# Kernel tuning notes

Hardware: AMD Instinct MI355X
Metric: run time of the kernel (lower is better)

Reference implementation:

```python
import jax, jax.numpy as jnp
import numpy as np

N, E, FIN, H, OUT, L = 80000, 1280000, 128, 64, 10, 3
NEG_SLOPE = 0.2


def setup_inputs() -> dict:
    key = jax.random.key(0)
    ks = jax.random.split(key, 2 + 6 * L + 2)
    inp = {
        "x": jax.random.normal(ks[0], (N, FIN), dtype=jnp.float32),
        "edge_index": jax.random.randint(ks[1], (2, E), 0, N, dtype=jnp.int32),
        "batch": jnp.zeros((N,), dtype=jnp.int32),
    }
    k = 2
    for l in range(L):
        fin = FIN if l == 0 else H
        s = 1.0 / np.sqrt(fin)
        inp[f"Wl{l}"] = jax.random.normal(ks[k + 0], (H, fin), dtype=jnp.float32) * s
        inp[f"bl{l}"] = jnp.zeros((H,), dtype=jnp.float32)
        inp[f"Wr{l}"] = jax.random.normal(ks[k + 1], (H, fin), dtype=jnp.float32) * s
        inp[f"br{l}"] = jnp.zeros((H,), dtype=jnp.float32)
        inp[f"att{l}"] = jax.random.normal(ks[k + 2], (H,), dtype=jnp.float32) * (1.0 / np.sqrt(H))
        inp[f"b{l}"] = jnp.zeros((H,), dtype=jnp.float32)
        k += 3
    inp["Wro"] = jax.random.normal(ks[k], (OUT, H), dtype=jnp.float32) * (1.0 / np.sqrt(H))
    inp["bro"] = jnp.zeros((OUT,), dtype=jnp.float32)
    return inp


def gatv2_layer(h, src, dst, Wl, bl, Wr, br, att, b):
    # PyG GATv2Conv (heads=1, share_weights=False):
    #   xl = lin_l(h) (source side), xr = lin_r(h) (target side)
    xl = h @ Wl.T + bl          # [N, H]
    xr = h @ Wr.T + br          # [N, H]
    e = jax.nn.leaky_relu(xl[src] + xr[dst], NEG_SLOPE) @ att  # [E_tot]
    # softmax over incoming edges of each destination node
    m = jax.ops.segment_max(e, dst, num_segments=N)
    ex = jnp.exp(e - m[dst])
    denom = jax.ops.segment_sum(ex, dst, num_segments=N)
    alpha = ex / denom[dst]
    out = jax.ops.segment_sum(alpha[:, None] * xl[src], dst, num_segments=N)
    return out + b


def reference(x, edge_index, batch,
              Wl0, bl0, Wr0, br0, att0, b0,
              Wl1, bl1, Wr1, br1, att1, b1,
              Wl2, bl2, Wr2, br2, att2, b2,
              Wro, bro):
    # add self-loops once (same augmented edge set used each layer)
    loop = jnp.arange(N, dtype=edge_index.dtype)
    src = jnp.concatenate([edge_index[0], loop])
    dst = jnp.concatenate([edge_index[1], loop])
    layers = [
        (Wl0, bl0, Wr0, br0, att0, b0),
        (Wl1, bl1, Wr1, br1, att1, b1),
        (Wl2, bl2, Wr2, br2, att2, b2),
    ]
    h = x
    for (Wl, bl, Wr, br, att, b) in layers:
        h = jax.nn.relu(gatv2_layer(h, src, dst, Wl, bl, Wr, br, att, b))
    # graph_level_task=False: node-level readout
    return h @ Wro.T + bro  # [N, OUT]
```

## Files before the change

kernel.cpp:

```cpp
#include <hip/hip_runtime.h>
#include <hip/hip_bf16.h>
#include <hip/hip_fp16.h>


#define NN 80000
#define EE 1280000
#define FIN 128
#define HH 64
#define OUTD 10
#define NBUK 79
#define PCH 2048
#define NCH 625

typedef __hip_bfloat16 bf16;

__device__ __forceinline__ float ldw(const void* p, int i, int f) {
    return f ? __bfloat162float(((const bf16*)p)[i]) : ((const float*)p)[i];
}

__global__ void detect_kernel(const unsigned* __restrict__ w, int* __restrict__ flag) {
    int lane = threadIdx.x;
    int big = 0;
    for (int i = lane; i < 2048; i += 64) {
        unsigned u = w[i];
        float a = __uint_as_float(u << 16);
        float b = __uint_as_float(u & 0xffff0000u);
        if (!(fabsf(a) <= 1024.f)) big = 1;
        if (!(fabsf(b) <= 1024.f)) big = 1;
    }
    big = (__ballot(big) != 0ull) ? 1 : 0;
    if (lane == 0) flag[0] = big ? 0 : 1;
}

__global__ void preconvert(
    const void* Wl0, const void* Wr0, const void* Wl1, const void* Wr1,
    const void* Wl2, const void* Wr2,
    const void* bl0, const void* br0, const void* bl1, const void* br1,
    const void* bl2, const void* br2,
    const void* att0, const void* att1, const void* att2,
    const void* b0, const void* b1, const void* b2,
    const void* Wro, const void* bro,
    float* WT0, float* WT1, float* WT2, float* small,
    const int* __restrict__ flagp)
{
    const int f = flagp[0];
    int t = blockIdx.x * 256 + threadIdx.x;
    if (t < 16384) {
        int j = t & 127, k = t >> 7;
        float v = (j < 64) ? ldw(Wl0, j * 128 + k, f) : ldw(Wr0, (j - 64) * 128 + k, f);
        WT0[k * 128 + j] = v;
    } else if (t < 24576) {
        int u = t - 16384; int j = u & 127, k = u >> 7;
        float v = (j < 64) ? ldw(Wl1, j * 64 + k, f) : ldw(Wr1, (j - 64) * 64 + k, f);
        WT1[k * 128 + j] = v;
    } else if (t < 32768) {
        int u = t - 24576; int j = u & 127, k = u >> 7;
        float v = (j < 64) ? ldw(Wl2, j * 64 + k, f) : ldw(Wr2, (j - 64) * 64 + k, f);
        WT2[k * 128 + j] = v;
    } else if (t < 34304) {
        int s = t - 32768;
        const void* BL[3] = { bl0, bl1, bl2 };
        const void* BR[3] = { br0, br1, br2 };
        const void* AT[3] = { att0, att1, att2 };
        const void* BB[3] = { b0, b1, b2 };
        float v = 0.f;
        if (s < 384) {
            int l = s / 128, r = s % 128;
            v = (r < 64) ? ldw(BL[l], r, f) : ldw(BR[l], r - 64, f);
        } else if (s < 576) {
            int q = s - 384; v = ldw(AT[q / 64], q % 64, f);
        } else if (s < 768) {
            int q = s - 576; v = ldw(BB[q / 64], q % 64, f);
        } else if (s < 1408) {
            v = ldw(Wro, s - 768, f);
        } else if (s < 1418) {
            v = ldw(bro, s - 1408, f);
        } else return;
        small[s] = v;
    }
}

__global__ __launch_bounds__(256) void chunkhist_kernel(const int* __restrict__ dst,
                                                        int* __restrict__ chunkcnt)
{
    __shared__ int h[NBUK];
    const int tid = threadIdx.x, c = blockIdx.x;
    for (int i = tid; i < NBUK; i += 256) h[i] = 0;
    __syncthreads();
    const int e0 = c * PCH + tid * 8;
    int4 a = *(const int4*)(dst + e0);
    int4 b = *(const int4*)(dst + e0 + 4);
    atomicAdd(&h[a.x >> 10], 1); atomicAdd(&h[a.y >> 10], 1);
    atomicAdd(&h[a.z >> 10], 1); atomicAdd(&h[a.w >> 10], 1);
    atomicAdd(&h[b.x >> 10], 1); atomicAdd(&h[b.y >> 10], 1);
    atomicAdd(&h[b.z >> 10], 1); atomicAdd(&h[b.w >> 10], 1);
    __syncthreads();
    for (int i = tid; i < NBUK; i += 256) chunkcnt[i * NCH + c] = h[i];
}

__global__ __launch_bounds__(1024) void cscan_kernel(int* __restrict__ chunkcnt,
                                                     int* __restrict__ bucket_cnt)
{
    __shared__ int s[1024];
    const int b = blockIdx.x, t = threadIdx.x;
    int v = (t < NCH) ? chunkcnt[b * NCH + t] : 0;
    s[t] = v;
    __syncthreads();
    #pragma unroll
    for (int off = 1; off < 1024; off <<= 1) {
        int u = (t >= off) ? s[t - off] : 0;
        __syncthreads();
        s[t] += u;
        __syncthreads();
    }
    if (t < NCH) chunkcnt[b * NCH + t] = s[t] - v;
    if (t == NCH - 1) bucket_cnt[b] = s[t];
}

__global__ void bscan_kernel(const int* __restrict__ bucket_cnt,
                             int* __restrict__ bucket_base)
{
    __shared__ int sc[128];
    const int t = threadIdx.x;
    sc[t] = (t < NBUK) ? bucket_cnt[t] : 0;
    __syncthreads();
    #pragma unroll
    for (int off = 1; off < 128; off <<= 1) {
        int v = (t >= off) ? sc[t - off] : 0;
        __syncthreads();
        sc[t] += v;
        __syncthreads();
    }
    if (t < NBUK) bucket_base[t] = (t == 0) ? 0 : sc[t - 1];
    if (t == 0) bucket_base[NBUK] = sc[NBUK - 1];
}

__global__ __launch_bounds__(256) void part_kernel(const int* __restrict__ src,
                                                   const int* __restrict__ dst,
                                                   const int* __restrict__ chunkcnt,
                                                   const int* __restrict__ bucket_base,
                                                   int2* __restrict__ part)
{
    __shared__ int hcnt[NBUK];
    __shared__ int sc[128];
    __shared__ int hbase[NBUK + 1];
    __shared__ int hpos[NBUK];
    __shared__ int hgb[NBUK];
    __shared__ int2 stage[PCH];
    const int tid = threadIdx.x, c = blockIdx.x;

    for (int i = tid; i < NBUK; i += 256) hcnt[i] = 0;
    __syncthreads();

    const int e0 = c * PCH + tid * 8;
    int4 sa = *(const int4*)(src + e0);
    int4 sb = *(const int4*)(src + e0 + 4);
    int4 da = *(const int4*)(dst + e0);
    int4 db = *(const int4*)(dst + e0 + 4);
    int dv[8] = { da.x, da.y, da.z, da.w, db.x, db.y, db.z, db.w };
    int sv[8] = { sa.x, sa.y, sa.z, sa.w, sb.x, sb.y, sb.z, sb.w };
    #pragma unroll
    for (int u = 0; u < 8; u++) atomicAdd(&hcnt[dv[u] >> 10], 1);
    __syncthreads();

    if (tid < 128) sc[tid] = (tid < NBUK) ? hcnt[tid] : 0;
    __syncthreads();
    #pragma unroll
    for (int off = 1; off < 128; off <<= 1) {
        int v = (tid < 128 && tid >= off) ? sc[tid - off] : 0;
        __syncthreads();
        if (tid < 128) sc[tid] += v;
        __syncthreads();
    }
    if (tid < NBUK) {
        int b = (tid == 0) ? 0 : sc[tid - 1];
        hbase[tid] = b;
        hpos[tid] = b;
        hgb[tid] = bucket_base[tid] + chunkcnt[tid * NCH + c];
    }
    if (tid == 0) hbase[NBUK] = PCH;
    __syncthreads();

    #pragma unroll
    for (int u = 0; u < 8; u++) {
        int p = atomicAdd(&hpos[dv[u] >> 10], 1);
        stage[p] = make_int2(sv[u], dv[u]);
    }
    __syncthreads();

    for (int s = tid; s < PCH; s += 256) {
        int lo = 0, hi = NBUK;
        #pragma unroll
        for (int it = 0; it < 7; it++) {
            int mid = (lo + hi) >> 1;
            if (hbase[mid] <= s) lo = mid; else hi = mid;
        }
        part[hgb[lo] + (s - hbase[lo])] = stage[s];
    }
}

__global__ __launch_bounds__(256) void hist_part_kernel(const int2* __restrict__ part,
                                                        const int* __restrict__ bucket_base,
                                                        int* __restrict__ cnt)
{
    __shared__ int lcnt[1024];
    const int b = blockIdx.x, tid = threadIdx.x;
    const int dbase = b << 10;
    for (int i = tid; i < 1024; i += 256) lcnt[i] = 0;
    __syncthreads();
    const int eb = bucket_base[b], ee = bucket_base[b + 1];
    for (int e = eb + tid; e < ee; e += 256)
        atomicAdd(&lcnt[part[e].y - dbase], 1);
    __syncthreads();
    const int nd = min(1024, NN - dbase);
    for (int i = tid; i < nd; i += 256) cnt[dbase + i] = lcnt[i];
}

__global__ void scan1(const int* __restrict__ cnt, int* __restrict__ rowptr,
                      int* __restrict__ bsums) {
    __shared__ int sh[256];
    int i = blockIdx.x * 256 + threadIdx.x;
    int tid = threadIdx.x;
    int c = (i < NN) ? cnt[i] : 0;
    sh[tid] = c;
    __syncthreads();
    #pragma unroll
    for (int off = 1; off < 256; off <<= 1) {
        int t = (tid >= off) ? sh[tid - off] : 0;
        __syncthreads();
        sh[tid] += t;
        __syncthreads();
    }
    if (i < NN) rowptr[i + 1] = sh[tid];
    if (tid == 255) bsums[blockIdx.x] = sh[255];
}

__global__ void scan2(int* __restrict__ bsums, int nb) {
    __shared__ int sh[512];
    int t = threadIdx.x;
    sh[t] = (t < nb) ? bsums[t] : 0;
    __syncthreads();
    #pragma unroll
    for (int off = 1; off < 512; off <<= 1) {
        int v = (t >= off) ? sh[t - off] : 0;
        __syncthreads();
        sh[t] += v;
        __syncthreads();
    }
    if (t < nb) bsums[t] = sh[t];
}

__global__ void scan3(int* __restrict__ rowptr, const int* __restrict__ bsums) {
    int i = blockIdx.x * 256 + threadIdx.x;
    if (i == 0) rowptr[0] = 0;
    int add = (blockIdx.x == 0) ? 0 : bsums[blockIdx.x - 1];
    if (i < NN) rowptr[i + 1] += add;
}

__global__ __launch_bounds__(256) void scatter2_kernel(const int2* __restrict__ part,
                                                       const int* __restrict__ bucket_base,
                                                       const int* __restrict__ rowptr,
                                                       int2* __restrict__ col2)
{
    __shared__ int lfill[1024];
    const int b = blockIdx.x, tid = threadIdx.x;
    const int dbase = b << 10;
    const int nd = min(1024, NN - dbase);
    for (int i = tid; i < nd; i += 256) lfill[i] = rowptr[dbase + i];
    __syncthreads();
    const int eb = bucket_base[b], ee = bucket_base[b + 1];
    for (int e = eb + tid; e < ee; e += 256) {
        int2 sd = part[e];
        int pos = atomicAdd(&lfill[sd.y - dbase], 1);
        col2[pos] = sd;
    }
}

template<int F, bool L0>
__global__ __launch_bounds__(256) void lin_fast(const void* __restrict__ hin_,
                                                const float* __restrict__ WT,
                                                const float* __restrict__ biasLR,
                                                __half* __restrict__ xlh,
                                                float* __restrict__ xr,
                                                const int* __restrict__ flagp)
{
    constexpr int LDR = 72;
    __shared__ __align__(16) float xs[F * LDR];
    const int t = threadIdx.x;
    const int nb = blockIdx.x * 64;

    if (L0 && flagp[0]) {
        const unsigned* hp = (const unsigned*)hin_;
        for (int idx = t; idx < 64 * (F / 2); idx += 256) {
            int r = idx / (F / 2), c = idx % (F / 2);
            unsigned u = hp[(size_t)(nb + r) * (F / 2) + c];
            xs[(2 * c) * LDR + r]     = __uint_as_float(u << 16);
            xs[(2 * c + 1) * LDR + r] = __uint_as_float(u & 0xffff0000u);
        }
    } else {
        const float* hp = (const float*)hin_;
        for (int idx = t; idx < 64 * F; idx += 256) {
            int r = idx / F, c = idx % F;
            xs[c * LDR + r] = hp[(size_t)(nb + r) * F + c];
        }
    }
    __syncthreads();

    const int c = t & 31;
    const int g = t >> 5;
    const float4* W4 = (const float4*)WT;
    const float4 bias = ((const float4*)biasLR)[c];
    float4 acc[8];
    #pragma unroll
    for (int u = 0; u < 8; u++) acc[u] = bias;

    #pragma unroll 2
    for (int k = 0; k < F; k++) {
        float4 w  = W4[k * 32 + c];
        float4 xa = *(const float4*)&xs[k * LDR + g * 8];
        float4 xb = *(const float4*)&xs[k * LDR + g * 8 + 4];
        acc[0].x = fmaf(xa.x, w.x, acc[0].x); acc[0].y = fmaf(xa.x, w.y, acc[0].y);
        acc[0].z = fmaf(xa.x, w.z, acc[0].z); acc[0].w = fmaf(xa.x, w.w, acc[0].w);
        acc[1].x = fmaf(xa.y, w.x, acc[1].x); acc[1].y = fmaf(xa.y, w.y, acc[1].y);
        acc[1].z = fmaf(xa.y, w.z, acc[1].z); acc[1].w = fmaf(xa.y, w.w, acc[1].w);
        acc[2].x = fmaf(xa.z, w.x, acc[2].x); acc[2].y = fmaf(xa.z, w.y, acc[2].y);
        acc[2].z = fmaf(xa.z, w.z, acc[2].z); acc[2].w = fmaf(xa.z, w.w, acc[2].w);
        acc[3].x = fmaf(xa.w, w.x, acc[3].x); acc[3].y = fmaf(xa.w, w.y, acc[3].y);
        acc[3].z = fmaf(xa.w, w.z, acc[3].z); acc[3].w = fmaf(xa.w, w.w, acc[3].w);
        acc[4].x = fmaf(xb.x, w.x, acc[4].x); acc[4].y = fmaf(xb.x, w.y, acc[4].y);
        acc[4].z = fmaf(xb.x, w.z, acc[4].z); acc[4].w = fmaf(xb.x, w.w, acc[4].w);
        acc[5].x = fmaf(xb.y, w.x, acc[5].x); acc[5].y = fmaf(xb.y, w.y, acc[5].y);
        acc[5].z = fmaf(xb.y, w.z, acc[5].z); acc[5].w = fmaf(xb.y, w.w, acc[5].w);
        acc[6].x = fmaf(xb.z, w.x, acc[6].x); acc[6].y = fmaf(xb.z, w.y, acc[6].y);
        acc[6].z = fmaf(xb.z, w.z, acc[6].z); acc[6].w = fmaf(xb.z, w.w, acc[6].w);
        acc[7].x = fmaf(xb.w, w.x, acc[7].x); acc[7].y = fmaf(xb.w, w.y, acc[7].y);
        acc[7].z = fmaf(xb.w, w.z, acc[7].z); acc[7].w = fmaf(xb.w, w.w, acc[7].w);
    }

    const int j0 = 4 * c;
    if (j0 < 64) {
        #pragma unroll
        for (int u = 0; u < 8; u++) {
            size_t row = nb + g * 8 + u;
            __half* xp = xlh + row * 64 + j0;
            *(__half2*)(xp)     = __floats2half2_rn(acc[u].x, acc[u].y);
            *(__half2*)(xp + 2) = __floats2half2_rn(acc[u].z, acc[u].w);
        }
    } else {
        #pragma unroll
        for (int u = 0; u < 8; u++) {
            size_t row = nb + g * 8 + u;
            *(float4*)(xr + row * 64 + (j0 - 64)) = acc[u];
        }
    }
}

#define DECODE8(U, D) { \
    float2 _f0 = __half22float2(*(__half2*)&U.x); \
    float2 _f1 = __half22float2(*(__half2*)&U.y); \
    float2 _f2 = __half22float2(*(__half2*)&U.z); \
    float2 _f3 = __half22float2(*(__half2*)&U.w); \
    D[0]=_f0.x; D[1]=_f0.y; D[2]=_f1.x; D[3]=_f1.y; \
    D[4]=_f2.x; D[5]=_f2.y; D[6]=_f3.x; D[7]=_f3.y; }

__global__ __launch_bounds__(256) void agg4_kernel(const __half* __restrict__ xlh,
                                                   const float* __restrict__ xr,
                                                   const float* __restrict__ attf,
                                                   const float* __restrict__ bf,
                                                   const int* __restrict__ rowptr,
                                                   const int2* __restrict__ col2,
                                                   float* __restrict__ hout)
{
    const int lane = threadIdx.x & 63;
    const int g = lane >> 3;
    const int r = lane & 7;
    int iw = blockIdx.x * 4 + (threadIdx.x >> 6);
    if (iw >= NN) return;
    const int i = __builtin_amdgcn_readfirstlane(iw);

    float xri[8], att[8];
    {
        float4 xa = *(const float4*)(xr + (size_t)i * 64 + r * 8);
        float4 xb = *(const float4*)(xr + (size_t)i * 64 + r * 8 + 4);
        xri[0]=xa.x; xri[1]=xa.y; xri[2]=xa.z; xri[3]=xa.w;
        xri[4]=xb.x; xri[5]=xb.y; xri[6]=xb.z; xri[7]=xb.w;
        float4 aa = *(const float4*)(attf + r * 8);
        float4 ab = *(const float4*)(attf + r * 8 + 4);
        att[0]=aa.x; att[1]=aa.y; att[2]=aa.z; att[3]=aa.w;
        att[4]=ab.x; att[5]=ab.y; att[6]=ab.z; att[7]=ab.w;
    }

    uint4 srow = *(const uint4*)(xlh + (size_t)i * 64 + r * 8);
    float s[8]; DECODE8(srow, s);
    float ps = 0.f;
    #pragma unroll
    for (int k = 0; k < 8; k++) {
        float u = s[k] + xri[k];
        ps = fmaf(att[k], fmaf(0.4f, fabsf(u), 0.6f * u), ps);
    }
    ps += __shfl_xor(ps, 1, 64);
    ps += __shfl_xor(ps, 2, 64);
    ps += __shfl_xor(ps, 4, 64);
    float wself = __expf(fminf(ps, 60.f));

    float acc[8];
    float denom;
    if (g == 0) {
        #pragma unroll
        for (int k = 0; k < 8; k++) acc[k] = wself * s[k];
        denom = wself;
    } else {
        #pragma unroll
        for (int k = 0; k < 8; k++) acc[k] = 0.f;
        denom = 0.f;
    }

    const int e0 = rowptr[i], e1 = rowptr[i + 1];
    const int n = e1 - e0;
    const int eL = e1 - 1;

    for (int base = 0; base < n; base += 16) {
        const int j = e0 + base;
        int sa = col2[min(j + g, eL)].x;
        int sb = col2[min(j + 8 + g, eL)].x;
        uint4 ua = *(const uint4*)(xlh + (size_t)sa * 64 + r * 8);
        uint4 ub = *(const uint4*)(xlh + (size_t)sb * 64 + r * 8);
        float A[8], B[8];
        DECODE8(ua, A);
        DECODE8(ub, B);

        float pa = 0.f, pb = 0.f;
        #pragma unroll
        for (int k = 0; k < 8; k++) {
            float va = A[k] + xri[k];
            float vb = B[k] + xri[k];
            pa = fmaf(att[k], fmaf(0.4f, fabsf(va), 0.6f * va), pa);
            pb = fmaf(att[k], fmaf(0.4f, fabsf(vb), 0.6f * vb), pb);
        }
        pa += __shfl_xor(pa, 1, 64);  pb += __shfl_xor(pb, 1, 64);
        pa += __shfl_xor(pa, 2, 64);  pb += __shfl_xor(pb, 2, 64);
        pa += __shfl_xor(pa, 4, 64);  pb += __shfl_xor(pb, 4, 64);

        float wa = (base + g < n)     ? __expf(fminf(pa, 60.f)) : 0.f;
        float wb = (base + 8 + g < n) ? __expf(fminf(pb, 60.f)) : 0.f;

        #pragma unroll
        for (int k = 0; k < 8; k++) {
            acc[k] = fmaf(wa, A[k], acc[k]);
            acc[k] = fmaf(wb, B[k], acc[k]);
        }
        denom += wa + wb;
    }

    #pragma unroll
    for (int off = 8; off < 64; off <<= 1) {
        #pragma unroll
        for (int k = 0; k < 8; k++) acc[k] += __shfl_xor(acc[k], off, 64);
        denom += __shfl_xor(denom, off, 64);
    }

    if (g == 0) {
        float inv = 1.f / denom;
        float4 bfa = *(const float4*)(bf + r * 8);
        float4 bfb = *(const float4*)(bf + r * 8 + 4);
        float o0 = fmaxf(fmaf(acc[0], inv, bfa.x), 0.f);
        float o1 = fmaxf(fmaf(acc[1], inv, bfa.y), 0.f);
        float o2 = fmaxf(fmaf(acc[2], inv, bfa.z), 0.f);
        float o3 = fmaxf(fmaf(acc[3], inv, bfa.w), 0.f);
        float o4 = fmaxf(fmaf(acc[4], inv, bfb.x), 0.f);
        float o5 = fmaxf(fmaf(acc[5], inv, bfb.y), 0.f);
        float o6 = fmaxf(fmaf(acc[6], inv, bfb.z), 0.f);
        float o7 = fmaxf(fmaf(acc[7], inv, bfb.w), 0.f);
        float* op = hout + (size_t)i * 64 + r * 8;
        *(float4*)(op)     = make_float4(o0, o1, o2, o3);
        *(float4*)(op + 4) = make_float4(o4, o5, o6, o7);
    }
}

__global__ __launch_bounds__(256) void readout2_kernel(const float* __restrict__ h,
                                                       const float* __restrict__ WROf,
                                                       const float* __restrict__ brof,
                                                       void* __restrict__ out,
                                                       const int* __restrict__ flagp)
{
    __shared__ float wsh[640];
    __shared__ float bsh[OUTD];
    const int tid = threadIdx.x;
    for (int idx = tid; idx < 640; idx += 256) {
        int k = idx / 10, o = idx % 10;
        wsh[idx] = WROf[o * 64 + k];
    }
    if (tid < OUTD) bsh[tid] = brof[tid];
    __syncthreads();

    const int i = blockIdx.x * 256 + tid;
    if (i >= NN) return;
    const int f = flagp[0];

    float res[OUTD];
    #pragma unroll
    for (int o = 0; o < OUTD; o++) res[o] = bsh[o];

    const float4* h4 = (const float4*)(h + (size_t)i * 64);
    #pragma unroll 4
    for (int c = 0; c < 16; c++) {
        float4 hv = h4[c];
        const float* wp = &wsh[c * 40];
        #pragma unroll
        for (int o = 0; o < OUTD; o++) {
            float t = fmaf(hv.x, wp[o], fmaf(hv.y, wp[10 + o],
                      fmaf(hv.z, wp[20 + o], hv.w * wp[30 + o])));
            res[o] += t;
        }
    }

    if (f) {
        bf16* op = (bf16*)out + (size_t)i * OUTD;
        #pragma unroll
        for (int o = 0; o < OUTD; o++) op[o] = __float2bfloat16(res[o]);
    } else {
        float* op = (float*)out + (size_t)i * OUTD;
        #pragma unroll
        for (int o = 0; o < OUTD; o++) op[o] = res[o];
    }
}

extern "C" void kernel_launch(void* const* d_in, const int* in_sizes, int n_in,
                              void* d_out, int out_size, void* d_ws, size_t ws_size,
                              hipStream_t stream) {
    const void* x   = d_in[0];
    const int* ei   = (const int*)d_in[1];
    const void* Wl0 = d_in[3];  const void* bl0 = d_in[4];
    const void* Wr0 = d_in[5];  const void* br0 = d_in[6];
    const void* at0 = d_in[7];  const void* b0  = d_in[8];
    const void* Wl1 = d_in[9];  const void* bl1 = d_in[10];
    const void* Wr1 = d_in[11]; const void* br1 = d_in[12];
    const void* at1 = d_in[13]; const void* b1  = d_in[14];
    const void* Wl2 = d_in[15]; const void* bl2 = d_in[16];
    const void* Wr2 = d_in[17]; const void* br2 = d_in[18];
    const void* at2 = d_in[19]; const void* b2  = d_in[20];
    const void* Wro = d_in[21]; const void* bro = d_in[22];

    const int* srcArr = ei;
    const int* dstArr = ei + EE;

    float* wf = (float*)d_ws;
    float* WT0   = wf;
    float* WT1   = wf + 16384;
    float* WT2   = wf + 24576;
    float* small = wf + 32768;
    int*   flag  = (int*)(wf + 34304);
    int*   rowptr = (int*)(wf + 34368);
    int*   bsums  = (int*)(wf + 114496);
    int*   fillc  = (int*)(wf + 115008);
    int*   bucket_cnt  = (int*)(wf + 195008);
    int*   bucket_base = (int*)(wf + 195136);
    int*   chunkcnt    = (int*)(wf + 195264);
    int2*  part   = (int2*)(wf + 244736);
    int2*  col2   = (int2*)(wf + 2804736);
    __half* xlh   = (__half*)(wf + 5364736);
    float* xr = wf + 7924736;
    float* hA = xr + (size_t)NN * 64;

    float* biasLR0 = small;        float* biasLR1 = small + 128; float* biasLR2 = small + 256;
    float* attf0 = small + 384;    float* attf1 = small + 448;   float* attf2 = small + 512;
    float* bf0   = small + 576;    float* bf1   = small + 640;   float* bf2   = small + 704;
    float* WROf  = small + 768;    float* brof  = small + 1408;

    detect_kernel<<<dim3(1), dim3(64), 0, stream>>>((const unsigned*)Wl0, flag);

    preconvert<<<dim3(134), dim3(256), 0, stream>>>(
        Wl0, Wr0, Wl1, Wr1, Wl2, Wr2, bl0, br0, bl1, br1, bl2, br2,
        at0, at1, at2, b0, b1, b2, Wro, bro, WT0, WT1, WT2, small, flag);

    chunkhist_kernel<<<dim3(NCH), dim3(256), 0, stream>>>(dstArr, chunkcnt);
    cscan_kernel<<<dim3(NBUK), dim3(1024), 0, stream>>>(chunkcnt, bucket_cnt);
    bscan_kernel<<<dim3(1), dim3(128), 0, stream>>>(bucket_cnt, bucket_base);
    part_kernel<<<dim3(NCH), dim3(256), 0, stream>>>(srcArr, dstArr, chunkcnt, bucket_base, part);
    hist_part_kernel<<<dim3(NBUK), dim3(256), 0, stream>>>(part, bucket_base, fillc);
    scan1<<<dim3(313), dim3(256), 0, stream>>>(fillc, rowptr, bsums);
    scan2<<<dim3(1), dim3(512), 0, stream>>>(bsums, 313);
    scan3<<<dim3(313), dim3(256), 0, stream>>>(rowptr, bsums);
    scatter2_kernel<<<dim3(NBUK), dim3(256), 0, stream>>>(part, bucket_base, rowptr, col2);

    lin_fast<128, true><<<dim3(NN / 64), dim3(256), 0, stream>>>(x, WT0, biasLR0, xlh, xr, flag);
    agg4_kernel<<<dim3(NN / 4), dim3(256), 0, stream>>>(xlh, xr, attf0, bf0, rowptr, col2, hA);
    lin_fast<64, false><<<dim3(NN / 64), dim3(256), 0, stream>>>(hA, WT1, biasLR1, xlh, xr, flag);
    agg4_kernel<<<dim3(NN / 4), dim3(256), 0, stream>>>(xlh, xr, attf1, bf1, rowptr, col2, hA);
    lin_fast<64, false><<<dim3(NN / 64), dim3(256), 0, stream>>>(hA, WT2, biasLR2, xlh, xr, flag);
    agg4_kernel<<<dim3(NN / 4), dim3(256), 0, stream>>>(xlh, xr, attf2, bf2, rowptr, col2, hA);

    readout2_kernel<<<dim3(313), dim3(256), 0, stream>>>(hA, WROf, brof, d_out, flag);
}
```

Baseline: 442.8 us.

## Replace FP32 FMA linear layers with FP16 MFMA matrix-core kernel

The per-layer dense projection (xl/xr) moves from a scalar FP32 FMA loop to MFMA 16x16x32 f16 instructions. Weights are preconverted to FP16 in row-major order. Activations are staged in LDS as FP16 with an XOR swizzle to avoid bank conflicts, and outputs go through an LDS epilogue for coalesced stores. This cuts ALU time in the GEMM phase, at the cost of FP16 rounding of inputs and weights, which could hurt accuracy.

```diff
diff --git a/kernel.cpp b/kernel.cpp
--- a/kernel.cpp
+++ b/kernel.cpp
@@ -13,6 +13,8 @@
 #define NCH 625
 
 typedef __hip_bfloat16 bf16;
+typedef _Float16 f16x8 __attribute__((ext_vector_type(8)));
+typedef float f32x4 __attribute__((ext_vector_type(4)));
 
 __device__ __forceinline__ float ldw(const void* p, int i, int f) {
     return f ? __bfloat162float(((const bf16*)p)[i]) : ((const float*)p)[i];
@@ -40,7 +42,7 @@
     const void* att0, const void* att1, const void* att2,
     const void* b0, const void* b1, const void* b2,
     const void* Wro, const void* bro,
-    float* WT0, float* WT1, float* WT2, float* small,
+    __half* Wh0, __half* Wh1, __half* Wh2, float* small,
     const int* __restrict__ flagp)
 {
     const int f = flagp[0];
@@ -48,15 +50,15 @@
     if (t < 16384) {
         int j = t & 127, k = t >> 7;
         float v = (j < 64) ? ldw(Wl0, j * 128 + k, f) : ldw(Wr0, (j - 64) * 128 + k, f);
-        WT0[k * 128 + j] = v;
+        Wh0[j * 128 + k] = __float2half(v);
     } else if (t < 24576) {
         int u = t - 16384; int j = u & 127, k = u >> 7;
         float v = (j < 64) ? ldw(Wl1, j * 64 + k, f) : ldw(Wr1, (j - 64) * 64 + k, f);
-        WT1[k * 128 + j] = v;
+        Wh1[j * 64 + k] = __float2half(v);
     } else if (t < 32768) {
         int u = t - 24576; int j = u & 127, k = u >> 7;
         float v = (j < 64) ? ldw(Wl2, j * 64 + k, f) : ldw(Wr2, (j - 64) * 64 + k, f);
-        WT2[k * 128 + j] = v;
+        Wh2[j * 64 + k] = __float2half(v);
     } else if (t < 34304) {
         int s = t - 32768;
         const void* BL[3] = { bl0, bl1, bl2 };
@@ -276,82 +278,100 @@
     }
 }
 
+#define ELX_S 72
+#define EXR_S 68
 template<int F, bool L0>
-__global__ __launch_bounds__(256) void lin_fast(const void* __restrict__ hin_,
-                                                const float* __restrict__ WT,
+__global__ __launch_bounds__(256) void lin_mfma(const void* __restrict__ hin_,
+                                                const __half* __restrict__ Wh,
                                                 const float* __restrict__ biasLR,
                                                 __half* __restrict__ xlh,
                                                 float* __restrict__ xr,
                                                 const int* __restrict__ flagp)
 {
-    constexpr int LDR = 72;
-    __shared__ __align__(16) float xs[F * LDR];
-    const int t = threadIdx.x;
+    __shared__ __align__(16) char lds[64 * ELX_S * 2 + 64 * EXR_S * 4];
+    _Float16* xs  = (_Float16*)lds;
+    _Float16* eXL = (_Float16*)lds;
+    float*    eXR = (float*)(lds + 64 * ELX_S * 2);
+
+    const int tid = threadIdx.x;
     const int nb = blockIdx.x * 64;
+    constexpr int OPR = F / 8;
 
     if (L0 && flagp[0]) {
-        const unsigned* hp = (const unsigned*)hin_;
-        for (int idx = t; idx < 64 * (F / 2); idx += 256) {
-            int r = idx / (F / 2), c = idx % (F / 2);
-            unsigned u = hp[(size_t)(nb + r) * (F / 2) + c];
-            xs[(2 * c) * LDR + r]     = __uint_as_float(u << 16);
-            xs[(2 * c + 1) * LDR + r] = __uint_as_float(u & 0xffff0000u);
+        const uint4* hp = (const uint4*)hin_;
+        for (int c = tid; c < 64 * OPR; c += 256) {
+            int row = c / OPR, oct = c % OPR;
+            uint4 u = hp[((size_t)(nb + row) * F + oct * 8) >> 3];
+            unsigned ww[4] = { u.x, u.y, u.z, u.w };
+            _Float16 v[8];
+            #pragma unroll
+            for (int p = 0; p < 4; p++) {
+                v[2 * p]     = (_Float16)__uint_as_float(ww[p] << 16);
+                v[2 * p + 1] = (_Float16)__uint_as_float(ww[p] & 0xffff0000u);
+            }
+            int so = oct ^ (row & 7);
+            *(f16x8*)&xs[row * F + so * 8] = *(f16x8*)v;
         }
     } else {
-        const float* hp = (const float*)hin_;
-        for (int idx = t; idx < 64 * F; idx += 256) {
-            int r = idx / F, c = idx % F;
-            xs[c * LDR + r] = hp[(size_t)(nb + r) * F + c];
-        }
-    }
-    __syncthreads();
-
-    const int c = t & 31;
-    const int g = t >> 5;
-    const float4* W4 = (const float4*)WT;
-    const float4 bias = ((const float4*)biasLR)[c];
-    float4 acc[8];
-    #pragma unroll
-    for (int u = 0; u < 8; u++) acc[u] = bias;
-
-    #pragma unroll 2
-    for (int k = 0; k < F; k++) {
-        float4 w  = W4[k * 32 + c];
-        float4 xa = *(const float4*)&xs[k * LDR + g * 8];
-        float4 xb = *(const float4*)&xs[k * LDR + g * 8 + 4];
-        acc[0].x = fmaf(xa.x, w.x, acc[0].x); acc[0].y = fmaf(xa.x, w.y, acc[0].y);
-        acc[0].z = fmaf(xa.x, w.z, acc[0].z); acc[0].w = fmaf(xa.x, w.w, acc[0].w);
-        acc[1].x = fmaf(xa.y, w.x, acc[1].x); acc[1].y = fmaf(xa.y, w.y, acc[1].y);
-        acc[1].z = fmaf(xa.y, w.z, acc[1].z); acc[1].w = fmaf(xa.y, w.w, acc[1].w);
-        acc[2].x = fmaf(xa.z, w.x, acc[2].x); acc[2].y = fmaf(xa.z, w.y, acc[2].y);
-        acc[2].z = fmaf(xa.z, w.z, acc[2].z); acc[2].w = fmaf(xa.z, w.w, acc[2].w);
-        acc[3].x = fmaf(xa.w, w.x, acc[3].x); acc[3].y = fmaf(xa.w, w.y, acc[3].y);
-        acc[3].z = fmaf(xa.w, w.z, acc[3].z); acc[3].w = fmaf(xa.w, w.w, acc[3].w);
-        acc[4].x = fmaf(xb.x, w.x, acc[4].x); acc[4].y = fmaf(xb.x, w.y, acc[4].y);
-        acc[4].z = fmaf(xb.x, w.z, acc[4].z); acc[4].w = fmaf(xb.x, w.w, acc[4].w);
-        acc[5].x = fmaf(xb.y, w.x, acc[5].x); acc[5].y = fmaf(xb.y, w.y, acc[5].y);
-        acc[5].z = fmaf(xb.y, w.z, acc[5].z); acc[5].w = fmaf(xb.y, w.w, acc[5].w);
-        acc[6].x = fmaf(xb.z, w.x, acc[6].x); acc[6].y = fmaf(xb.z, w.y, acc[6].y);
-        acc[6].z = fmaf(xb.z, w.z, acc[6].z); acc[6].w = fmaf(xb.z, w.w, acc[6].w);
-        acc[7].x = fmaf(xb.w, w.x, acc[7].x); acc[7].y = fmaf(xb.w, w.y, acc[7].y);
-        acc[7].z = fmaf(xb.w, w.z, acc[7].z); acc[7].w = fmaf(xb.w, w.w, acc[7].w);
-    }
-
-    const int j0 = 4 * c;
-    if (j0 < 64) {
-        #pragma unroll
-        for (int u = 0; u < 8; u++) {
-            size_t row = nb + g * 8 + u;
-            __half* xp = xlh + row * 64 + j0;
-            *(__half2*)(xp)     = __floats2half2_rn(acc[u].x, acc[u].y);
-            *(__half2*)(xp + 2) = __floats2half2_rn(acc[u].z, acc[u].w);
-        }
-    } else {
-        #pragma unroll
-        for (int u = 0; u < 8; u++) {
-            size_t row = nb + g * 8 + u;
-            *(float4*)(xr + row * 64 + (j0 - 64)) = acc[u];
-        }
+        const float4* hp = (const float4*)hin_;
+        for (int c = tid; c < 64 * OPR; c += 256) {
+            int row = c / OPR, oct = c % OPR;
+            size_t base = ((size_t)(nb + row) * F + oct * 8) >> 2;
+            float4 a = hp[base], b = hp[base + 1];
+            _Float16 v[8] = { (_Float16)a.x, (_Float16)a.y, (_Float16)a.z, (_Float16)a.w,
+                              (_Float16)b.x, (_Float16)b.y, (_Float16)b.z, (_Float16)b.w };
+            int so = oct ^ (row & 7);
+            *(f16x8*)&xs[row * F + so * 8] = *(f16x8*)v;
+        }
+    }
+    __syncthreads();
+
+    const int w = tid >> 6;
+    const int lane = tid & 63;
+    const int n = lane & 15;
+    const int quad = lane >> 4;
+    constexpr int NS = F / 32;
+
+    f16x8 afr[NS];
+    #pragma unroll
+    for (int s = 0; s < NS; s++) {
+        int o = (s * 4 + quad) ^ (n & 7);
+        afr[s] = *(const f16x8*)&xs[(w * 16 + n) * F + o * 8];
+    }
+    __syncthreads();
+
+    const _Float16* Whf = (const _Float16*)Wh;
+    #pragma unroll
+    for (int ct = 0; ct < 8; ct++) {
+        float bv = biasLR[ct * 16 + n];
+        f32x4 acc = { bv, bv, bv, bv };
+        #pragma unroll
+        for (int s = 0; s < NS; s++) {
+            f16x8 bfr = *(const f16x8*)&Whf[(size_t)(ct * 16 + n) * F + s * 32 + quad * 8];
+            acc = __builtin_amdgcn_mfma_f32_16x16x32_f16(afr[s], bfr, acc, 0, 0, 0);
+        }
+        int rbase = w * 16 + quad * 4;
+        if (ct < 4) {
+            #pragma unroll
+            for (int rg = 0; rg < 4; rg++)
+                eXL[(rbase + rg) * ELX_S + ct * 16 + n] = (_Float16)acc[rg];
+        } else {
+            #pragma unroll
+            for (int rg = 0; rg < 4; rg++)
+                eXR[(rbase + rg) * EXR_S + (ct - 4) * 16 + n] = acc[rg];
+        }
+    }
+    __syncthreads();
+
+    for (int c = tid; c < 512; c += 256) {
+        int row = c >> 3, oct = c & 7;
+        *(uint4*)&xlh[(size_t)(nb + row) * 64 + oct * 8] =
+            *(const uint4*)&eXL[row * ELX_S + oct * 8];
+    }
+    for (int c = tid; c < 1024; c += 256) {
+        int row = c >> 4, q4 = c & 15;
+        *(float4*)&xr[(size_t)(nb + row) * 64 + q4 * 4] =
+            *(const float4*)&eXR[row * EXR_S + q4 * 4];
     }
 }
 
@@ -545,9 +565,9 @@
     const int* dstArr = ei + EE;
 
     float* wf = (float*)d_ws;
-    float* WT0   = wf;
-    float* WT1   = wf + 16384;
-    float* WT2   = wf + 24576;
+    __half* Wh0  = (__half*)wf;
+    __half* Wh1  = (__half*)(wf + 16384);
+    __half* Wh2  = (__half*)(wf + 24576);
     float* small = wf + 32768;
     int*   flag  = (int*)(wf + 34304);
     int*   rowptr = (int*)(wf + 34368);
@@ -571,7 +591,7 @@
 
     preconvert<<<dim3(134), dim3(256), 0, stream>>>(
         Wl0, Wr0, Wl1, Wr1, Wl2, Wr2, bl0, br0, bl1, br1, bl2, br2,
-        at0, at1, at2, b0, b1, b2, Wro, bro, WT0, WT1, WT2, small, flag);
+        at0, at1, at2, b0, b1, b2, Wro, bro, Wh0, Wh1, Wh2, small, flag);
 
     chunkhist_kernel<<<dim3(NCH), dim3(256), 0, stream>>>(dstArr, chunkcnt);
     cscan_kernel<<<dim3(NBUK), dim3(1024), 0, stream>>>(chunkcnt, bucket_cnt);
@@ -583,11 +603,11 @@
     scan3<<<dim3(313), dim3(256), 0, stream>>>(rowptr, bsums);
     scatter2_kernel<<<dim3(NBUK), dim3(256), 0, stream>>>(part, bucket_base, rowptr, col2);
 
-    lin_fast<128, true><<<dim3(NN / 64), dim3(256), 0, stream>>>(x, WT0, biasLR0, xlh, xr, flag);
+    lin_mfma<128, true><<<dim3(NN / 64), dim3(256), 0, stream>>>(x, Wh0, biasLR0, xlh, xr, flag);
     agg4_kernel<<<dim3(NN / 4), dim3(256), 0, stream>>>(xlh, xr, attf0, bf0, rowptr, col2, hA);
-    lin_fast<64, false><<<dim3(NN / 64), dim3(256), 0, stream>>>(hA, WT1, biasLR1, xlh, xr, flag);
+    lin_mfma<64, false><<<dim3(NN / 64), dim3(256), 0, stream>>>(hA, Wh1, biasLR1, xlh, xr, flag);
     agg4_kernel<<<dim3(NN / 4), dim3(256), 0, stream>>>(xlh, xr, attf1, bf1, rowptr, col2, hA);
-    lin_fast<64, false><<<dim3(NN / 64), dim3(256), 0, stream>>>(hA, WT2, biasLR2, xlh, xr, flag);
+    lin_mfma<64, false><<<dim3(NN / 64), dim3(256), 0, stream>>>(hA, Wh2, biasLR2, xlh, xr, flag);
     agg4_kernel<<<dim3(NN / 4), dim3(256), 0, stream>>>(xlh, xr, attf2, bf2, rowptr, col2, hA);
 
     readout2_kernel<<<dim3(313), dim3(256), 0, stream>>>(hA, WROf, brof, d_out, flag);
```

New measurement: 410.8 us. 1.08x faster.
